# Kernel tuning notes

Hardware: AMD Instinct MI355X
Metric: run time of the kernel (lower is better)

Reference implementation:

```python
import jax, jax.numpy as jnp
import numpy as np

N, P, D, C = 2048, 64, 512, 32   # bs*n_vars, patch_num, hidden_dim, cluster_num
H, DFF, L = 8, 2048, 3           # heads, ffn dim, encoder layers
TEMP = 10.0
EPS = 1e-10
LN_EPS = 1e-5


def setup_inputs() -> dict:
    key = jax.random.key(0)
    ks = jax.random.split(key, 18)
    s = 0.02  # small init to keep activations sane
    inp = {}
    inp["input_series"] = jax.random.normal(ks[0], (N, P, D), jnp.float32)
    pi = jax.random.uniform(ks[1], (C,), jnp.float32) + 0.1
    inp["text_pi"] = pi / pi.sum()
    A = jax.random.uniform(ks[2], (C, C), jnp.float32) + 0.1
    inp["text_A"] = A / A.sum(axis=1, keepdims=True)
    # stacked per-layer TransformerEncoderLayer params (torch post-norm, relu)
    inp["qkv_w"] = jax.random.normal(ks[3], (L, 3 * D, D), jnp.float32) * s
    inp["qkv_b"] = jnp.zeros((L, 3 * D), jnp.float32)
    inp["out_w"] = jax.random.normal(ks[4], (L, D, D), jnp.float32) * s
    inp["out_b"] = jnp.zeros((L, D), jnp.float32)
    inp["ln1_w"] = jnp.ones((L, D), jnp.float32)
    inp["ln1_b"] = jnp.zeros((L, D), jnp.float32)
    inp["ff1_w"] = jax.random.normal(ks[5], (L, DFF, D), jnp.float32) * s
    inp["ff1_b"] = jnp.zeros((L, DFF), jnp.float32)
    inp["ff2_w"] = jax.random.normal(ks[6], (L, D, DFF), jnp.float32) * s
    inp["ff2_b"] = jnp.zeros((L, D), jnp.float32)
    inp["ln2_w"] = jnp.ones((L, D), jnp.float32)
    inp["ln2_b"] = jnp.zeros((L, D), jnp.float32)
    inp["mus"] = jax.random.normal(ks[7], (C, D), jnp.float32)
    return inp


def _layer_norm(x, w, b):
    m = x.mean(axis=-1, keepdims=True)
    v = ((x - m) ** 2).mean(axis=-1, keepdims=True)
    return (x - m) * jax.lax.rsqrt(v + LN_EPS) * w + b


def _encoder_layer(x, qkv_w, qkv_b, out_w, out_b, ln1_w, ln1_b,
                   ff1_w, ff1_b, ff2_w, ff2_b, ln2_w, ln2_b):
    n, p, d = x.shape
    dh = d // H
    qkv = x @ qkv_w.T + qkv_b                       # [n,p,3d]
    q, k, v = jnp.split(qkv, 3, axis=-1)
    def split_heads(t):
        return t.reshape(n, p, H, dh).transpose(0, 2, 1, 3)  # [n,h,p,dh]
    q, k, v = split_heads(q), split_heads(k), split_heads(v)
    scores = jnp.einsum('nhqd,nhkd->nhqk', q, k) / (dh ** 0.5)
    attn = jax.nn.softmax(scores, axis=-1)
    o = jnp.einsum('nhqk,nhkd->nhqd', attn, v)
    o = o.transpose(0, 2, 1, 3).reshape(n, p, d)
    o = o @ out_w.T + out_b
    x = _layer_norm(x + o, ln1_w, ln1_b)            # post-norm
    f = jax.nn.relu(x @ ff1_w.T + ff1_b) @ ff2_w.T + ff2_b
    return _layer_norm(x + f, ln2_w, ln2_b)


def reference(input_series, text_pi, text_A, qkv_w, qkv_b, out_w, out_b,
              ln1_w, ln1_b, ff1_w, ff1_b, ff2_w, ff2_b, ln2_w, ln2_b, mus):
    x = input_series
    for l in range(L):
        x = _encoder_layer(x, qkv_w[l], qkv_b[l], out_w[l], out_b[l],
                           ln1_w[l], ln1_b[l], ff1_w[l], ff1_b[l],
                           ff2_w[l], ff2_b[l], ln2_w[l], ln2_b[l])
    emb_ts = x                                       # [N,P,D]
    # ClusterCenters: softmax of exp(-||x - tanh(mu)||^2 / T)
    mu = jnp.tanh(mus)                               # [C,D]
    dist = ((emb_ts ** 2).sum(-1)[..., None]
            + (mu ** 2).sum(-1)[None, None, :]
            - 2.0 * jnp.einsum('npd,cd->npc', emb_ts, mu))  # [N,P,C]
    z = jnp.exp(-dist / TEMP)
    logits_all = z / z.sum(axis=-1, keepdims=True)
    log_za = jnp.log(logits_all + EPS)               # [N,P,C]
    # sequential HMM-style recursion over patches
    l0 = jax.nn.softmax(jnp.log(text_pi + EPS)[None, :] + log_za[:, 0], axis=-1)
    def step(c, lz):
        c2 = jax.nn.softmax(jnp.log(c @ text_A + EPS) + lz, axis=-1)
        return c2, c2
    _, ys = jax.lax.scan(step, l0, jnp.swapaxes(log_za[:, 1:], 0, 1))  # [P-1,N,C]
    cluster_probs = jnp.concatenate([l0[:, None], jnp.swapaxes(ys, 0, 1)], axis=1)
    entropy_loss = -jnp.sum(cluster_probs * jnp.log(cluster_probs + EPS), axis=-1).mean()
    return (cluster_probs, emb_ts, text_pi, text_A, entropy_loss)
```

## Files before the change

kernel.cpp:

```cpp
#include <hip/hip_runtime.h>
#include <stdint.h>


typedef __bf16 bf16;
typedef __bf16 bf16x2 __attribute__((ext_vector_type(2)));
typedef __bf16 bf16x4 __attribute__((ext_vector_type(4)));
typedef __bf16 bf16x8 __attribute__((ext_vector_type(8)));
typedef float  f32x4  __attribute__((ext_vector_type(4)));
typedef float  f32x2  __attribute__((ext_vector_type(2)));

#define EPSF 1e-10f
#define NROWS 131072L

__device__ __forceinline__ float bflo(uint32_t u){ return __uint_as_float(u << 16); }
__device__ __forceinline__ float bfhi(uint32_t u){ return __uint_as_float(u & 0xffff0000u); }

__device__ __forceinline__ void gload_lds16(const bf16* g, bf16* l){
  __builtin_amdgcn_global_load_lds((const __attribute__((address_space(1))) uint32_t*)g,
                                   (__attribute__((address_space(3))) uint32_t*)l,
                                   16, 0, 0);
}

__global__ void k_f2bf(const float* __restrict__ in, bf16* __restrict__ out, long n){
  const long stride = (long)gridDim.x * blockDim.x * 4;
  for (long i = ((long)blockIdx.x * blockDim.x + threadIdx.x) * 4; i < n; i += stride){
    f32x4 v = *(const f32x4*)(in + i);
    bf16x4 o = { (bf16)v[0], (bf16)v[1], (bf16)v[2], (bf16)v[3] };
    *(bf16x4*)(out + i) = o;
  }
}


#define MFMA_PH(SM, SN)                                                       \
  {                                                                           \
    __builtin_amdgcn_s_setprio(1);                                            \
    _Pragma("unroll")                                                         \
    for (int kk = 0; kk < 2; kk++) {                                          \
      _Pragma("unroll")                                                       \
      for (int i2 = 0; i2 < 4; i2++) {                                        \
        _Pragma("unroll")                                                     \
        for (int j2 = 0; j2 < 2; j2++) {                                      \
          acc[(SM)*4+i2][(SN)*2+j2] = __builtin_amdgcn_mfma_f32_16x16x32_bf16(\
              a[i2][kk], b[SN][j2][kk], acc[(SM)*4+i2][(SN)*2+j2], 0, 0, 0);  \
        }                                                                     \
      }                                                                       \
    }                                                                         \
    __builtin_amdgcn_s_setprio(0);                                            \
  }

#define RD_A(SM)                                                              \
  _Pragma("unroll")                                                           \
  for (int i2 = 0; i2 < 4; i2++) {                                            \
    a[i2][0] = *(const bf16x8*)&Ac[(SM)*8192 + aBase + i2*1024 + sl0];        \
    a[i2][1] = *(const bf16x8*)&Ac[(SM)*8192 + aBase + i2*1024 + sl1];        \
  }

#define RD_B(SN)                                                              \
  _Pragma("unroll")                                                           \
  for (int j2 = 0; j2 < 2; j2++) {                                            \
    b[SN][j2][0] = *(const bf16x8*)&Bc[(SN)*8192 + bBase + j2*1024 + sl0];    \
    b[SN][j2][1] = *(const bf16x8*)&Bc[(SN)*8192 + bBase + j2*1024 + sl1];    \
  }

#define ISSUE_A(dst, RO, KK) \
  gload_lds16(gA + (long)(RO)*lda + (KK), (dst) + (RO)*64 + wsl)
#define ISSUE_B(dst, RO, KK) \
  gload_lds16(gB + (long)(RO)*K   + (KK), (dst) + (RO)*64 + wsl)

#define WAITV(N)  asm volatile("s_waitcnt vmcnt(" #N ")" ::: "memory")
#define WAITL0    asm volatile("s_waitcnt lgkmcnt(0)" ::: "memory")
#define BARRIER   { __builtin_amdgcn_s_barrier(); asm volatile("" ::: "memory"); }

template<int RELU>
__global__ __launch_bounds__(512, 2)
void gemm256(const bf16* __restrict__ A, long lda,
             const bf16* __restrict__ W,
             const float* __restrict__ bias,
             bf16* __restrict__ Cb, long K, int nbx)
{
  const int tid  = threadIdx.x;
  const int wid  = tid >> 6;
  const int lane = tid & 63;
  const int wr = wid >> 2, wc = wid & 3;
  const long ldc = (long)nbx * 256;

  const unsigned nwg = gridDim.x;
  const unsigned q   = nwg >> 3;
  const unsigned swz = (blockIdx.x & 7) * q + (blockIdx.x >> 3);
  const unsigned bx  = swz % (unsigned)nbx;
  const unsigned by  = swz / (unsigned)nbx;
  const long bm = (long)by * 256;
  const long bn = (long)bx * 256;

  __shared__ __align__(16) bf16 smem[65536];
  bf16* const As0 = smem;
  bf16* const Bs0 = smem + 16384;
  bf16* const As1 = smem + 32768;
  bf16* const Bs1 = smem + 49152;

  const int gswz = ((lane & 7) ^ ((lane >> 3) & 7)) * 8;
  const int wsl  = wid * 512;
  const bf16* gA = A + (bm + wid * 8 + (lane >> 3)) * lda + gswz;
  const bf16* gB = W + (bn + wid * 8 + (lane >> 3)) * K   + gswz;

  const int fr = lane & 15, fg = lane >> 4;
  const int aBase = (wr * 64 + fr) * 64;
  const int bBase = (wc * 32 + fr) * 64;
  const int sl0 = ((0 + fg) ^ (fr & 7)) * 8;
  const int sl1 = ((4 + fg) ^ (fr & 7)) * 8;

  f32x4 acc[8][4];
#pragma unroll
  for (int i = 0; i < 8; i++)
#pragma unroll
    for (int j = 0; j < 4; j++) acc[i][j] = (f32x4){0.f, 0.f, 0.f, 0.f};

  bf16x8 a[4][2];
  bf16x8 b[2][2][2];

  const int nt = (int)(K >> 6);

  ISSUE_A(As0, 0, 0);   ISSUE_A(As0, 64, 0);
  ISSUE_B(Bs0, 0, 0);   ISSUE_B(Bs0, 64, 0);
  ISSUE_A(As0, 128, 0); ISSUE_A(As0, 192, 0);
  ISSUE_B(Bs0, 128, 0); ISSUE_B(Bs0, 192, 0);
  if (nt > 1){
    ISSUE_A(As1, 0, 64); ISSUE_A(As1, 64, 64);
    ISSUE_B(Bs1, 0, 64); ISSUE_B(Bs1, 64, 64);
  }
  WAITV(8);
  BARRIER;

  for (int t = 0; t < nt; t++){
    bf16* const Ac = (t & 1) ? As1 : As0;
    bf16* const Bc = (t & 1) ? Bs1 : Bs0;
    bf16* const An = (t & 1) ? As0 : As1;
    bf16* const Bn = (t & 1) ? Bs0 : Bs1;
    const bool s1 = (t + 1 < nt);
    const bool s2 = (t + 2 < nt);
    const long kn  = (long)(t + 1) << 6;
    const long kn2 = (long)(t + 2) << 6;

    RD_A(0); RD_B(0);
    if (s1){ ISSUE_A(An, 128, kn); ISSUE_A(An, 192, kn); }
    WAITL0;
    MFMA_PH(0, 0);
    if (s1){ WAITV(6); } else { WAITV(0); }
    BARRIER;

    RD_B(1);
    if (s1){ ISSUE_B(Bn, 128, kn); ISSUE_B(Bn, 192, kn); }
    WAITL0;
    MFMA_PH(0, 1);
    BARRIER;

    RD_A(1);
    if (s2){ ISSUE_A(Ac, 0, kn2); ISSUE_A(Ac, 64, kn2); }
    WAITL0;
    MFMA_PH(1, 0);
    BARRIER;

    if (s2){ ISSUE_B(Bc, 0, kn2); ISSUE_B(Bc, 64, kn2); }
    MFMA_PH(1, 1);
    if (s2)      { WAITV(8); }
    else if (s1) { WAITV(4); }
    BARRIER;
  }

  bf16* const cw = smem + wid * 1280;
  float bv[4];
#pragma unroll
  for (int sn = 0; sn < 2; sn++)
#pragma unroll
    for (int j2 = 0; j2 < 2; j2++)
      bv[sn * 2 + j2] = bias[bn + sn * 128 + wc * 32 + j2 * 16 + fr];

#pragma unroll
  for (int sm = 0; sm < 2; sm++){
#pragma unroll
    for (int sn = 0; sn < 2; sn++){
#pragma unroll
      for (int ch = 0; ch < 2; ch++){
#pragma unroll
        for (int i2 = 0; i2 < 2; i2++){
#pragma unroll
          for (int j2 = 0; j2 < 2; j2++){
#pragma unroll
            for (int r = 0; r < 4; r++){
              float v = acc[sm * 4 + ch * 2 + i2][sn * 2 + j2][r] + bv[sn * 2 + j2];
              if (RELU) v = fmaxf(v, 0.f);
              cw[(i2 * 16 + fg * 4 + r) * 40 + j2 * 16 + fr] = (bf16)v;
            }
          }
        }
        WAITL0;
        const long r0 = bm + sm * 128 + wr * 64 + ch * 32;
        const long c0 = bn + sn * 128 + wc * 32;
#pragma unroll
        for (int p = 0; p < 2; p++){
          const int row = p * 16 + (lane >> 2);
          const int colg = (lane & 3) * 8;
          bf16x8 o = *(const bf16x8*)&cw[row * 40 + colg];
          *(bf16x8*)&Cb[(r0 + row) * ldc + c0 + colg] = o;
        }
        WAITL0;
      }
    }
  }
}

__global__ __launch_bounds__(256)
void attention(bf16* __restrict__ qkv)
{
  const int blk = blockIdx.x;
  const long n = blk >> 3;
  const int h  = blk & 7;
  const int tid = threadIdx.x;
  const int wid = tid >> 6, lane = tid & 63;

  __shared__ __align__(16) bf16 Qs[64][72];
  __shared__ __align__(16) bf16 Ks[64][72];
  __shared__ __align__(16) bf16 Vt[64][72];

  bf16* base = qkv + n * 64 * 1536 + h * 64;

  for (int c = tid; c < 512; c += 256){
    const int row = c >> 3, col = (c & 7) * 8;
    const long go = (long)row * 1536 + col;
    *(bf16x8*)&Qs[row][col] = *(const bf16x8*)(base + go);
    *(bf16x8*)&Ks[row][col] = *(const bf16x8*)(base + 512 + go);
    bf16x8 v = *(const bf16x8*)(base + 1024 + go);
#pragma unroll
    for (int e = 0; e < 8; e++) Vt[col + e][row] = v[e];
  }
  __syncthreads();

  const int fr = lane & 15, fg = lane >> 4;
  f32x4 sacc[4];
#pragma unroll
  for (int j = 0; j < 4; j++) sacc[j] = (f32x4){0.f, 0.f, 0.f, 0.f};
#pragma unroll
  for (int ks = 0; ks < 2; ks++){
    bf16x8 aa = *(const bf16x8*)&Qs[wid * 16 + fr][ks * 32 + fg * 8];
#pragma unroll
    for (int j = 0; j < 4; j++){
      bf16x8 bb = *(const bf16x8*)&Ks[j * 16 + fr][ks * 32 + fg * 8];
      sacc[j] = __builtin_amdgcn_mfma_f32_16x16x32_bf16(aa, bb, sacc[j], 0, 0, 0);
    }
  }

  float pv[4][4];
#pragma unroll
  for (int r = 0; r < 4; r++){
    float m = -1e30f;
#pragma unroll
    for (int j = 0; j < 4; j++) m = fmaxf(m, sacc[j][r]);
#pragma unroll
    for (int msk = 1; msk < 16; msk <<= 1) m = fmaxf(m, __shfl_xor(m, msk));
    float s = 0.f;
#pragma unroll
    for (int j = 0; j < 4; j++){
      float p = __expf((sacc[j][r] - m) * 0.125f);
      pv[j][r] = p; s += p;
    }
#pragma unroll
    for (int msk = 1; msk < 16; msk <<= 1) s += __shfl_xor(s, msk);
    const float inv = 1.f / s;
#pragma unroll
    for (int j = 0; j < 4; j++) pv[j][r] *= inv;
  }

#pragma unroll
  for (int j = 0; j < 4; j++)
#pragma unroll
    for (int r = 0; r < 4; r++)
      Qs[wid * 16 + fg * 4 + r][j * 16 + fr] = (bf16)pv[j][r];
  __syncthreads();

  f32x4 oacc[4];
#pragma unroll
  for (int j = 0; j < 4; j++) oacc[j] = (f32x4){0.f, 0.f, 0.f, 0.f};
#pragma unroll
  for (int ks = 0; ks < 2; ks++){
    bf16x8 aa = *(const bf16x8*)&Qs[wid * 16 + fr][ks * 32 + fg * 8];
#pragma unroll
    for (int j = 0; j < 4; j++){
      bf16x8 bb = *(const bf16x8*)&Vt[j * 16 + fr][ks * 32 + fg * 8];
      oacc[j] = __builtin_amdgcn_mfma_f32_16x16x32_bf16(aa, bb, oacc[j], 0, 0, 0);
    }
  }
#pragma unroll
  for (int j = 0; j < 4; j++)
#pragma unroll
    for (int r = 0; r < 4; r++)
      base[(long)(wid * 16 + fg * 4 + r) * 1536 + j * 16 + fr] = (bf16)oacc[j][r];
}

__global__ __launch_bounds__(256)
void resid_ln(const bf16* __restrict__ X, const bf16* __restrict__ O,
              const float* __restrict__ w, const float* __restrict__ b,
              bf16* __restrict__ Y, float* __restrict__ EF)
{
  const int wid = threadIdx.x >> 6, lane = threadIdx.x & 63;
  const long row = (long)blockIdx.x * 4 + wid;
  const uint4 xu = ((const uint4*)(X + row * 512))[lane];
  const uint4 ou = ((const uint4*)(O + row * 512))[lane];
  float s[8];
  s[0] = bflo(xu.x) + bflo(ou.x);  s[1] = bfhi(xu.x) + bfhi(ou.x);
  s[2] = bflo(xu.y) + bflo(ou.y);  s[3] = bfhi(xu.y) + bfhi(ou.y);
  s[4] = bflo(xu.z) + bflo(ou.z);  s[5] = bfhi(xu.z) + bfhi(ou.z);
  s[6] = bflo(xu.w) + bflo(ou.w);  s[7] = bfhi(xu.w) + bfhi(ou.w);
  float sum = 0.f, sq = 0.f;
#pragma unroll
  for (int e = 0; e < 8; e++){ sum += s[e]; sq += s[e] * s[e]; }
#pragma unroll
  for (int m = 1; m < 64; m <<= 1){ sum += __shfl_xor(sum, m); sq += __shfl_xor(sq, m); }
  const float mean = sum * (1.f / 512.f);
  const float var  = sq * (1.f / 512.f) - mean * mean;
  const float rs   = rsqrtf(var + 1e-5f);
  const f32x4 w0 = *(const f32x4*)(w + 8 * lane);
  const f32x4 w1 = *(const f32x4*)(w + 8 * lane + 4);
  const f32x4 b0 = *(const f32x4*)(b + 8 * lane);
  const f32x4 b1 = *(const f32x4*)(b + 8 * lane + 4);
  float o[8];
#pragma unroll
  for (int e = 0; e < 4; e++) o[e]     = (s[e]     - mean) * rs * w0[e] + b0[e];
#pragma unroll
  for (int e = 0; e < 4; e++) o[e + 4] = (s[e + 4] - mean) * rs * w1[e] + b1[e];
  bf16x8 ov = { (bf16)o[0], (bf16)o[1], (bf16)o[2], (bf16)o[3],
                (bf16)o[4], (bf16)o[5], (bf16)o[6], (bf16)o[7] };
  *(bf16x8*)(Y + row * 512 + 8 * lane) = ov;
  if (EF){
    f32x4 e0 = { o[0], o[1], o[2], o[3] };
    f32x4 e1 = { o[4], o[5], o[6], o[7] };
    *(f32x4*)(EF + row * 512 + 8 * lane) = e0;
    *(f32x4*)(EF + row * 512 + 8 * lane + 4) = e1;
  }
}

__global__ __launch_bounds__(256)
void k_mu(const float* __restrict__ mus, bf16* __restrict__ mubf, float* __restrict__ munorm)
{
  const int c = blockIdx.x, tid = threadIdx.x, lane = tid & 63, wid = tid >> 6;
  const f32x2 v = *(const f32x2*)(mus + c * 512 + 2 * tid);
  const float t0 = tanhf(v[0]), t1 = tanhf(v[1]);
  bf16x2 o2 = { (bf16)t0, (bf16)t1 };
  *(bf16x2*)(mubf + c * 512 + 2 * tid) = o2;
  float sq = t0 * t0 + t1 * t1;
#pragma unroll
  for (int m = 1; m < 64; m <<= 1) sq += __shfl_xor(sq, m);
  __shared__ float red[4];
  if (lane == 0) red[wid] = sq;
  __syncthreads();
  if (tid == 0) munorm[c] = red[0] + red[1] + red[2] + red[3];
}

__global__ __launch_bounds__(256)
void cluster_logza(const bf16* __restrict__ X, const bf16* __restrict__ MU,
                   const float* __restrict__ munorm, float* __restrict__ out)
{
  const int tid = threadIdx.x, lane = tid & 63, wid = tid >> 6;
  __shared__ __align__(16) bf16 mus[32][512];
  __shared__ float xs[512];
  __shared__ float red[4];
  __shared__ float dots[32];
  for (int c = tid; c < 2048; c += 256){
    const int r = c >> 6, col = (c & 63) * 8;
    *(bf16x8*)&mus[r][col] = *(const bf16x8*)(MU + r * 512 + col);
  }
  const int cc = tid >> 3, seg = tid & 7;
  const long row0 = (long)blockIdx.x * 16;
  __syncthreads();
  for (int rr = 0; rr < 16; rr++){
    const long row = row0 + rr;
    const uint32_t u = ((const uint32_t*)(X + row * 512))[tid];
    const float aa = bflo(u), bb = bfhi(u);
    xs[2 * tid] = aa; xs[2 * tid + 1] = bb;
    float sq = aa * aa + bb * bb;
#pragma unroll
    for (int m = 1; m < 64; m <<= 1) sq += __shfl_xor(sq, m);
    if (lane == 0) red[wid] = sq;
    __syncthreads();
    const float xn = red[0] + red[1] + red[2] + red[3];
    float p = 0.f;
#pragma unroll
    for (int jj = 0; jj < 8; jj++){
      const int col = jj * 64 + seg * 8;
      bf16x8 m8 = *(const bf16x8*)&mus[cc][col];
      const float* xv = &xs[col];
#pragma unroll
      for (int e = 0; e < 8; e++) p += xv[e] * (float)m8[e];
    }
#pragma unroll
    for (int m = 1; m < 8; m <<= 1) p += __shfl_xor(p, m);
    if (seg == 0) dots[cc] = p;
    __syncthreads();
    if (tid < 32){
      const float dist = xn + munorm[tid] - 2.f * dots[tid];
      const float lg = -dist * 0.1f;
      float mx = lg;
#pragma unroll
      for (int m = 1; m < 32; m <<= 1) mx = fmaxf(mx, __shfl_xor(mx, m, 32));
      const float z = __expf(lg - mx);
      float s = z;
#pragma unroll
      for (int m = 1; m < 32; m <<= 1) s += __shfl_xor(s, m, 32);
      out[row * 32 + tid] = logf(z / s + EPSF);
    }
    __syncthreads();
  }
}

__global__ __launch_bounds__(256)
void k_hmm(const float* __restrict__ lza, const float* __restrict__ pi,
           const float* __restrict__ A, float* __restrict__ cp, float* __restrict__ ent)
{
  __shared__ float As[32][33];
  const int tid = threadIdx.x;
  for (int i = tid; i < 1024; i += 256) As[i >> 5][i & 31] = A[i];
  __syncthreads();
  const int j = tid & 31;
  const long n = (long)blockIdx.x * 8 + (tid >> 5);
  const float* lz = lza + n * 2048;

  float c = logf(pi[j] + EPSF) + lz[j];
  {
    float mx = c;
#pragma unroll
    for (int m = 1; m < 32; m <<= 1) mx = fmaxf(mx, __shfl_xor(mx, m, 32));
    float z = __expf(c - mx), s = z;
#pragma unroll
    for (int m = 1; m < 32; m <<= 1) s += __shfl_xor(s, m, 32);
    c = z / s;
  }
  cp[n * 2048 + j] = c;
  float ea = -c * logf(c + EPSF);

  for (int p = 1; p < 64; p++){
    float y = 0.f;
#pragma unroll
    for (int i = 0; i < 32; i++) y += __shfl(c, i, 32) * As[i][j];
    float t = logf(y + EPSF) + lz[p * 32 + j];
    float mx = t;
#pragma unroll
    for (int m = 1; m < 32; m <<= 1) mx = fmaxf(mx, __shfl_xor(mx, m, 32));
    float z = __expf(t - mx), s = z;
#pragma unroll
    for (int m = 1; m < 32; m <<= 1) s += __shfl_xor(s, m, 32);
    c = z / s;
    cp[n * 2048 + p * 32 + j] = c;
    ea += -c * logf(c + EPSF);
  }
#pragma unroll
  for (int m = 1; m < 32; m <<= 1) ea += __shfl_xor(ea, m, 32);
  if (j == 0) atomicAdd(ent, ea * (1.f / 131072.f));
}

extern "C" void kernel_launch(void* const* d_in, const int* in_sizes, int n_in,
                              void* d_out, int out_size, void* d_ws, size_t ws_size,
                              hipStream_t stream)
{
  (void)in_sizes; (void)n_in; (void)out_size; (void)ws_size;
  const float* in_series = (const float*)d_in[0];
  const float* pi    = (const float*)d_in[1];
  const float* Amat  = (const float*)d_in[2];
  const float* qkv_w = (const float*)d_in[3];
  const float* qkv_b = (const float*)d_in[4];
  const float* out_w = (const float*)d_in[5];
  const float* out_b = (const float*)d_in[6];
  const float* ln1_w = (const float*)d_in[7];
  const float* ln1_b = (const float*)d_in[8];
  const float* ff1_w = (const float*)d_in[9];
  const float* ff1_b = (const float*)d_in[10];
  const float* ff2_w = (const float*)d_in[11];
  const float* ff2_b = (const float*)d_in[12];
  const float* ln2_w = (const float*)d_in[13];
  const float* ln2_b = (const float*)d_in[14];
  const float* mus   = (const float*)d_in[15];

  char* ws = (char*)d_ws;
  bf16* region0 = (bf16*)(ws);
  bf16* xb      = (bf16*)(ws + 536870912L);
  bf16* oproj   = (bf16*)(ws + 671088640L);
  bf16* w_qkv   = (bf16*)(ws + 805306368L);
  bf16* w_out   = (bf16*)(ws + 810024960L);
  bf16* w_ff1   = (bf16*)(ws + 811597824L);
  bf16* w_ff2   = (bf16*)(ws + 817889280L);
  bf16* mubf    = (bf16*)(ws + 824180736L);
  float* munorm = (float*)(ws + 824213504L);
  float* logza  = (float*)(ws);

  float* out_f = (float*)d_out;
  float* cp    = out_f;
  float* emb   = out_f + 4194304L;
  float* o_pi  = out_f + 71303168L;
  float* o_A   = out_f + 71303200L;
  float* o_ent = out_f + 71304224L;

  k_f2bf<<<8192, 256, 0, stream>>>(in_series, xb, 67108864L);
  k_f2bf<<<1024, 256, 0, stream>>>(qkv_w, w_qkv, 2359296L);
  k_f2bf<<<1024, 256, 0, stream>>>(out_w, w_out, 786432L);
  k_f2bf<<<1024, 256, 0, stream>>>(ff1_w, w_ff1, 3145728L);
  k_f2bf<<<1024, 256, 0, stream>>>(ff2_w, w_ff2, 3145728L);
  k_mu<<<32, 256, 0, stream>>>(mus, mubf, munorm);

  for (int l = 0; l < 3; l++){
    gemm256<0><<<3072, 512, 0, stream>>>(xb, 512, w_qkv + (long)l * 786432L,
                                         qkv_b + (long)l * 1536, region0, 512, 6);
    attention<<<16384, 256, 0, stream>>>(region0);
    gemm256<0><<<1024, 512, 0, stream>>>(region0, 1536, w_out + (long)l * 262144L,
                                         out_b + (long)l * 512, oproj, 512, 2);
    resid_ln<<<32768, 256, 0, stream>>>(xb, oproj, ln1_w + (long)l * 512,
                                        ln1_b + (long)l * 512, xb, nullptr);
    gemm256<1><<<4096, 512, 0, stream>>>(xb, 512, w_ff1 + (long)l * 1048576L,
                                         ff1_b + (long)l * 2048, region0, 512, 8);
    gemm256<0><<<1024, 512, 0, stream>>>(region0, 2048, w_ff2 + (long)l * 1048576L,
                                         ff2_b + (long)l * 512, oproj, 2048, 2);
    resid_ln<<<32768, 256, 0, stream>>>(xb, oproj, ln2_w + (long)l * 512,
                                        ln2_b + (long)l * 512, xb,
                                        (l == 2) ? emb : nullptr);
  }

  cluster_logza<<<8192, 256, 0, stream>>>(xb, mubf, munorm, logza);
  hipMemsetAsync(o_ent, 0, 4, stream);
  k_hmm<<<256, 256, 0, stream>>>(logza, pi, Amat, cp, o_ent);
  hipMemcpyAsync(o_pi, pi, 32 * sizeof(float), hipMemcpyDeviceToDevice, stream);
  hipMemcpyAsync(o_A, Amat, 1024 * sizeof(float), hipMemcpyDeviceToDevice, stream);
}
```

Before: 3.934 ms.

## Process two M tiles per GEMM block and fuse residual add into epilogue

Each GEMM workgroup now computes two consecutive 256-row tiles against the same 256-column weight tile. It streams both K-loops through one continuous pipeline and writes the first tile's epilogue midway, which halves the grid size and keeps the software pipeline full across the tile boundary. The out-proj and FF2 GEMMs now add the residual in their epilogue, so the following layer-norm kernel reads a single input instead of two. In exchange the kernel uses more shared memory for a dedicated epilogue staging area, which may reduce occupancy. The residual is also now rounded to bf16 before layer-norm, where previously the sum was done in fp32.

```diff
diff --git a/kernel.cpp b/kernel.cpp
--- a/kernel.cpp
+++ b/kernel.cpp
@@ -62,21 +62,65 @@
     b[SN][j2][1] = *(const bf16x8*)&Bc[(SN)*8192 + bBase + j2*1024 + sl1];    \
   }
 
-#define ISSUE_A(dst, RO, KK) \
-  gload_lds16(gA + (long)(RO)*lda + (KK), (dst) + (RO)*64 + wsl)
-#define ISSUE_B(dst, RO, KK) \
-  gload_lds16(gB + (long)(RO)*K   + (KK), (dst) + (RO)*64 + wsl)
-
 #define WAITV(N)  asm volatile("s_waitcnt vmcnt(" #N ")" ::: "memory")
 #define WAITL0    asm volatile("s_waitcnt lgkmcnt(0)" ::: "memory")
 #define BARRIER   { __builtin_amdgcn_s_barrier(); asm volatile("" ::: "memory"); }
 
-template<int RELU>
+#define ZERO_ACC                                                              \
+  _Pragma("unroll") for (int zi = 0; zi < 8; zi++)                            \
+  _Pragma("unroll") for (int zj = 0; zj < 4; zj++)                            \
+    acc[zi][zj] = (f32x4){0.f, 0.f, 0.f, 0.f};
+
+#define EPILOGUE(BME)                                                         \
+{                                                                             \
+  _Pragma("unroll")                                                           \
+  for (int sm = 0; sm < 2; sm++){                                             \
+    _Pragma("unroll")                                                         \
+    for (int sn = 0; sn < 2; sn++){                                           \
+      _Pragma("unroll")                                                       \
+      for (int ch = 0; ch < 2; ch++){                                         \
+        _Pragma("unroll")                                                     \
+        for (int i2 = 0; i2 < 2; i2++){                                       \
+          _Pragma("unroll")                                                   \
+          for (int j2 = 0; j2 < 2; j2++){                                     \
+            _Pragma("unroll")                                                 \
+            for (int r = 0; r < 4; r++){                                      \
+              float v = acc[sm*4 + ch*2 + i2][sn*2 + j2][r] + bv[sn*2 + j2];  \
+              if (RELU) v = fmaxf(v, 0.f);                                    \
+              cw[(i2*16 + fg*4 + r)*40 + j2*16 + fr] = (bf16)v;               \
+            }                                                                 \
+          }                                                                   \
+        }                                                                     \
+        WAITL0;                                                               \
+        const long r0 = (BME) + sm*128 + wr*64 + ch*32;                       \
+        const long c0 = bn + sn*128 + wc*32;                                  \
+        _Pragma("unroll")                                                     \
+        for (int p = 0; p < 2; p++){                                          \
+          const int row  = p*16 + (lane >> 2);                                \
+          const int colg = (lane & 3)*8;                                      \
+          bf16x8 o = *(const bf16x8*)&cw[row*40 + colg];                      \
+          if (HASRES){                                                        \
+            bf16x8 rs8 = *(const bf16x8*)&RES[(r0+row)*ldc + c0 + colg];      \
+            _Pragma("unroll")                                                 \
+            for (int e = 0; e < 8; e++)                                       \
+              o[e] = (bf16)((float)o[e] + (float)rs8[e]);                     \
+          }                                                                   \
+          *(bf16x8*)&Cb[(r0+row)*ldc + c0 + colg] = o;                        \
+        }                                                                     \
+        WAITL0;                                                               \
+      }                                                                       \
+    }                                                                         \
+  }                                                                           \
+}
+
+template<int RELU, int HASRES>
 __global__ __launch_bounds__(512, 2)
 void gemm256(const bf16* __restrict__ A, long lda,
              const bf16* __restrict__ W,
              const float* __restrict__ bias,
-             bf16* __restrict__ Cb, long K, int nbx)
+             bf16* __restrict__ Cb,
+             const bf16* __restrict__ RES,
+             long K, int nbx)
 {
   const int tid  = threadIdx.x;
   const int wid  = tid >> 6;
@@ -89,19 +133,21 @@
   const unsigned swz = (blockIdx.x & 7) * q + (blockIdx.x >> 3);
   const unsigned bx  = swz % (unsigned)nbx;
   const unsigned by  = swz / (unsigned)nbx;
-  const long bm = (long)by * 256;
-  const long bn = (long)bx * 256;
-
-  __shared__ __align__(16) bf16 smem[65536];
+  const long bm0 = (long)by * 512;
+  const long bn  = (long)bx * 256;
+
+  __shared__ __align__(16) bf16 smem[75776];
   bf16* const As0 = smem;
   bf16* const Bs0 = smem + 16384;
   bf16* const As1 = smem + 32768;
   bf16* const Bs1 = smem + 49152;
+  bf16* const cw  = smem + 65536 + wid * 1280;
 
   const int gswz = ((lane & 7) ^ ((lane >> 3) & 7)) * 8;
   const int wsl  = wid * 512;
-  const bf16* gA = A + (bm + wid * 8 + (lane >> 3)) * lda + gswz;
-  const bf16* gB = W + (bn + wid * 8 + (lane >> 3)) * K   + gswz;
+  const bf16* gA0 = A + (bm0 + wid * 8 + (lane >> 3)) * lda + gswz;
+  const bf16* gA1 = gA0 + 256 * lda;
+  const bf16* gB  = W + (bn + wid * 8 + (lane >> 3)) * K + gswz;
 
   const int fr = lane & 15, fg = lane >> 4;
   const int aBase = (wr * 64 + fr) * 64;
@@ -109,104 +155,81 @@
   const int sl0 = ((0 + fg) ^ (fr & 7)) * 8;
   const int sl1 = ((4 + fg) ^ (fr & 7)) * 8;
 
+  const int nt = (int)(K >> 6);
+  const int T  = nt * 2;
+
+  auto issueA = [&](bf16* dst, int ro, int tt){
+    const bf16* g = (tt >= nt) ? gA1 : gA0;
+    const long kk = (long)(tt >= nt ? tt - nt : tt) << 6;
+    gload_lds16(g + (long)ro * lda + kk, dst + ro * 64 + wsl);
+  };
+  auto issueB = [&](bf16* dst, int ro, int tt){
+    const long kk = (long)(tt >= nt ? tt - nt : tt) << 6;
+    gload_lds16(gB + (long)ro * K + kk, dst + ro * 64 + wsl);
+  };
+
   f32x4 acc[8][4];
-#pragma unroll
-  for (int i = 0; i < 8; i++)
-#pragma unroll
-    for (int j = 0; j < 4; j++) acc[i][j] = (f32x4){0.f, 0.f, 0.f, 0.f};
+  ZERO_ACC;
 
   bf16x8 a[4][2];
   bf16x8 b[2][2][2];
 
-  const int nt = (int)(K >> 6);
-
-  ISSUE_A(As0, 0, 0);   ISSUE_A(As0, 64, 0);
-  ISSUE_B(Bs0, 0, 0);   ISSUE_B(Bs0, 64, 0);
-  ISSUE_A(As0, 128, 0); ISSUE_A(As0, 192, 0);
-  ISSUE_B(Bs0, 128, 0); ISSUE_B(Bs0, 192, 0);
-  if (nt > 1){
-    ISSUE_A(As1, 0, 64); ISSUE_A(As1, 64, 64);
-    ISSUE_B(Bs1, 0, 64); ISSUE_B(Bs1, 64, 64);
-  }
+  float bv[4];
+#pragma unroll
+  for (int sn = 0; sn < 2; sn++)
+#pragma unroll
+    for (int j2 = 0; j2 < 2; j2++)
+      bv[sn * 2 + j2] = bias[bn + sn * 128 + wc * 32 + j2 * 16 + fr];
+
+  issueA(As0, 0, 0);   issueA(As0, 64, 0);
+  issueB(Bs0, 0, 0);   issueB(Bs0, 64, 0);
+  issueA(As0, 128, 0); issueA(As0, 192, 0);
+  issueB(Bs0, 128, 0); issueB(Bs0, 192, 0);
+  issueA(As1, 0, 1);   issueA(As1, 64, 1);
+  issueB(Bs1, 0, 1);   issueB(Bs1, 64, 1);
   WAITV(8);
   BARRIER;
 
-  for (int t = 0; t < nt; t++){
+  for (int t = 0; t < T; t++){
     bf16* const Ac = (t & 1) ? As1 : As0;
     bf16* const Bc = (t & 1) ? Bs1 : Bs0;
     bf16* const An = (t & 1) ? As0 : As1;
     bf16* const Bn = (t & 1) ? Bs0 : Bs1;
-    const bool s1 = (t + 1 < nt);
-    const bool s2 = (t + 2 < nt);
-    const long kn  = (long)(t + 1) << 6;
-    const long kn2 = (long)(t + 2) << 6;
+    const bool s1 = (t + 1 < T);
+    const bool s2 = (t + 2 < T);
 
     RD_A(0); RD_B(0);
-    if (s1){ ISSUE_A(An, 128, kn); ISSUE_A(An, 192, kn); }
+    if (s1){ issueA(An, 128, t + 1); issueA(An, 192, t + 1); }
     WAITL0;
     MFMA_PH(0, 0);
     if (s1){ WAITV(6); } else { WAITV(0); }
     BARRIER;
 
     RD_B(1);
-    if (s1){ ISSUE_B(Bn, 128, kn); ISSUE_B(Bn, 192, kn); }
+    if (s1){ issueB(Bn, 128, t + 1); issueB(Bn, 192, t + 1); }
     WAITL0;
     MFMA_PH(0, 1);
     BARRIER;
 
     RD_A(1);
-    if (s2){ ISSUE_A(Ac, 0, kn2); ISSUE_A(Ac, 64, kn2); }
+    if (s2){ issueA(Ac, 0, t + 2); issueA(Ac, 64, t + 2); }
     WAITL0;
     MFMA_PH(1, 0);
     BARRIER;
 
-    if (s2){ ISSUE_B(Bc, 0, kn2); ISSUE_B(Bc, 64, kn2); }
+    if (s2){ issueB(Bc, 0, t + 2); issueB(Bc, 64, t + 2); }
     MFMA_PH(1, 1);
     if (s2)      { WAITV(8); }
     else if (s1) { WAITV(4); }
     BARRIER;
-  }
-
-  bf16* const cw = smem + wid * 1280;
-  float bv[4];
-#pragma unroll
-  for (int sn = 0; sn < 2; sn++)
-#pragma unroll
-    for (int j2 = 0; j2 < 2; j2++)
-      bv[sn * 2 + j2] = bias[bn + sn * 128 + wc * 32 + j2 * 16 + fr];
-
-#pragma unroll
-  for (int sm = 0; sm < 2; sm++){
-#pragma unroll
-    for (int sn = 0; sn < 2; sn++){
-#pragma unroll
-      for (int ch = 0; ch < 2; ch++){
-#pragma unroll
-        for (int i2 = 0; i2 < 2; i2++){
-#pragma unroll
-          for (int j2 = 0; j2 < 2; j2++){
-#pragma unroll
-            for (int r = 0; r < 4; r++){
-              float v = acc[sm * 4 + ch * 2 + i2][sn * 2 + j2][r] + bv[sn * 2 + j2];
-              if (RELU) v = fmaxf(v, 0.f);
-              cw[(i2 * 16 + fg * 4 + r) * 40 + j2 * 16 + fr] = (bf16)v;
-            }
-          }
-        }
-        WAITL0;
-        const long r0 = bm + sm * 128 + wr * 64 + ch * 32;
-        const long c0 = bn + sn * 128 + wc * 32;
-#pragma unroll
-        for (int p = 0; p < 2; p++){
-          const int row = p * 16 + (lane >> 2);
-          const int colg = (lane & 3) * 8;
-          bf16x8 o = *(const bf16x8*)&cw[row * 40 + colg];
-          *(bf16x8*)&Cb[(r0 + row) * ldc + c0 + colg] = o;
-        }
-        WAITL0;
-      }
+
+    if (t == nt - 1){
+      EPILOGUE(bm0);
+      ZERO_ACC;
     }
   }
+
+  EPILOGUE(bm0 + 256);
 }
 
 __global__ __launch_bounds__(256)
@@ -297,19 +320,18 @@
 }
 
 __global__ __launch_bounds__(256)
-void resid_ln(const bf16* __restrict__ X, const bf16* __restrict__ O,
-              const float* __restrict__ w, const float* __restrict__ b,
-              bf16* __restrict__ Y, float* __restrict__ EF)
+void ln_only(const bf16* __restrict__ S,
+             const float* __restrict__ w, const float* __restrict__ b,
+             bf16* __restrict__ Y, float* __restrict__ EF)
 {
   const int wid = threadIdx.x >> 6, lane = threadIdx.x & 63;
   const long row = (long)blockIdx.x * 4 + wid;
-  const uint4 xu = ((const uint4*)(X + row * 512))[lane];
-  const uint4 ou = ((const uint4*)(O + row * 512))[lane];
+  const uint4 su = ((const uint4*)(S + row * 512))[lane];
   float s[8];
-  s[0] = bflo(xu.x) + bflo(ou.x);  s[1] = bfhi(xu.x) + bfhi(ou.x);
-  s[2] = bflo(xu.y) + bflo(ou.y);  s[3] = bfhi(xu.y) + bfhi(ou.y);
-  s[4] = bflo(xu.z) + bflo(ou.z);  s[5] = bfhi(xu.z) + bfhi(ou.z);
-  s[6] = bflo(xu.w) + bflo(ou.w);  s[7] = bfhi(xu.w) + bfhi(ou.w);
+  s[0] = bflo(su.x);  s[1] = bfhi(su.x);
+  s[2] = bflo(su.y);  s[3] = bfhi(su.y);
+  s[4] = bflo(su.z);  s[5] = bfhi(su.z);
+  s[6] = bflo(su.w);  s[7] = bfhi(su.w);
   float sum = 0.f, sq = 0.f;
 #pragma unroll
   for (int e = 0; e < 8; e++){ sum += s[e]; sq += s[e] * s[e]; }
@@ -505,20 +527,24 @@
   k_mu<<<32, 256, 0, stream>>>(mus, mubf, munorm);
 
   for (int l = 0; l < 3; l++){
-    gemm256<0><<<3072, 512, 0, stream>>>(xb, 512, w_qkv + (long)l * 786432L,
-                                         qkv_b + (long)l * 1536, region0, 512, 6);
+    gemm256<0,0><<<1536, 512, 0, stream>>>(xb, 512, w_qkv + (long)l * 786432L,
+                                           qkv_b + (long)l * 1536, region0, nullptr,
+                                           512, 6);
     attention<<<16384, 256, 0, stream>>>(region0);
-    gemm256<0><<<1024, 512, 0, stream>>>(region0, 1536, w_out + (long)l * 262144L,
-                                         out_b + (long)l * 512, oproj, 512, 2);
-    resid_ln<<<32768, 256, 0, stream>>>(xb, oproj, ln1_w + (long)l * 512,
-                                        ln1_b + (long)l * 512, xb, nullptr);
-    gemm256<1><<<4096, 512, 0, stream>>>(xb, 512, w_ff1 + (long)l * 1048576L,
-                                         ff1_b + (long)l * 2048, region0, 512, 8);
-    gemm256<0><<<1024, 512, 0, stream>>>(region0, 2048, w_ff2 + (long)l * 1048576L,
-                                         ff2_b + (long)l * 512, oproj, 2048, 2);
-    resid_ln<<<32768, 256, 0, stream>>>(xb, oproj, ln2_w + (long)l * 512,
-                                        ln2_b + (long)l * 512, xb,
-                                        (l == 2) ? emb : nullptr);
+    gemm256<0,1><<<512, 512, 0, stream>>>(region0, 1536, w_out + (long)l * 262144L,
+                                          out_b + (long)l * 512, oproj, xb,
+                                          512, 2);
+    ln_only<<<32768, 256, 0, stream>>>(oproj, ln1_w + (long)l * 512,
+                                       ln1_b + (long)l * 512, xb, nullptr);
+    gemm256<1,0><<<2048, 512, 0, stream>>>(xb, 512, w_ff1 + (long)l * 1048576L,
+                                           ff1_b + (long)l * 2048, region0, nullptr,
+                                           512, 8);
+    gemm256<0,1><<<512, 512, 0, stream>>>(region0, 2048, w_ff2 + (long)l * 1048576L,
+                                          ff2_b + (long)l * 512, oproj, xb,
+                                          2048, 2);
+    ln_only<<<32768, 256, 0, stream>>>(oproj, ln2_w + (long)l * 512,
+                                       ln2_b + (long)l * 512, xb,
+                                       (l == 2) ? emb : nullptr);
   }
 
   cluster_logza<<<8192, 256, 0, stream>>>(xb, mubf, munorm, logza);
```

After: 4.061 ms. 1.03x slower.
